# Kernel optimization log

Hardware: AMD Instinct MI355X
Metric: run time of the kernel (lower is better)

The kernel has to match this reference:

```python
import jax, jax.numpy as jnp
import numpy as np

N_NODES = 100000
N_EDGES = 1600000
IN_C = 64
HID = 64


def _glorot(key, shape):
    fan_in, fan_out = shape[1], shape[0]
    lim = (6.0 / (fan_in + fan_out)) ** 0.5
    return jax.random.uniform(key, shape, jnp.float32, -lim, lim)


def setup_inputs() -> dict:
    key = jax.random.key(0)
    ks = jax.random.split(key, 8)
    x = jax.random.normal(ks[0], (N_NODES, IN_C), jnp.float32)
    edge_index = jax.random.randint(ks[1], (2, N_EDGES), 0, N_NODES, jnp.int32)
    return {
        "x": x,
        "edge_index": edge_index,
        # conv1 (SAGEConv in->hid): lin_l (bias), lin_r (no bias)
        "W1l": _glorot(ks[2], (HID, IN_C)),
        "b1l": jnp.zeros((HID,), jnp.float32),
        "W1r": _glorot(ks[3], (HID, IN_C)),
        # conv2 (SAGEConv hid->hid)
        "W2l": _glorot(ks[4], (HID, HID)),
        "b2l": jnp.zeros((HID,), jnp.float32),
        "W2r": _glorot(ks[5], (HID, HID)),
        # edge scorer: Linear(2*hid, 1)
        "Wlin": _glorot(ks[6], (1, 2 * HID)),
        "blin": jnp.zeros((1,), jnp.float32),
    }


def _sage_conv(x, src, dst, Wl, bl, Wr, n_nodes):
    # mean aggregation of source features onto destination nodes
    agg = jax.ops.segment_sum(x[src], dst, num_segments=n_nodes)  # [N, F]
    cnt = jax.ops.segment_sum(jnp.ones((src.shape[0],), x.dtype), dst,
                              num_segments=n_nodes)  # [N]
    mean = agg / jnp.maximum(cnt, 1.0)[:, None]  # isolated nodes -> 0
    return mean @ Wl.T + bl + x @ Wr.T


def reference(x, edge_index, W1l, b1l, W1r, W2l, b2l, W2r, Wlin, blin):
    src, dst = edge_index[0], edge_index[1]
    n = x.shape[0]
    h = jax.nn.relu(_sage_conv(x, src, dst, W1l, b1l, W1r, n))
    h = jax.nn.relu(_sage_conv(h, src, dst, W2l, b2l, W2r, n))
    he = jnp.concatenate([h[src], h[dst]], axis=1)  # [E, 2*HID]
    return (he @ Wlin.T + blin).squeeze(-1)  # [E]
```

## Files before the change

### kernel.cpp

```cpp
#include <hip/hip_runtime.h>
#include <hip/hip_bf16.h>

#define N_NODES 100000
#define N_EDGES 1600000
#define NBUCK 196
#define BCAP 12288
#define CHUNK 4096
#define PART_BLOCKS 391


typedef __hip_bfloat16 bf16;
typedef short short8 __attribute__((ext_vector_type(8)));
typedef float f32x4 __attribute__((ext_vector_type(4)));
typedef unsigned int uint;

__device__ __forceinline__ short f2bs(float f) {
    bf16 h = __float2bfloat16(f);
    short s; __builtin_memcpy(&s, &h, 2); return s;
}
__device__ __forceinline__ float lo_bf(uint w) {
    uint v = w << 16; float f; __builtin_memcpy(&f, &v, 4); return f;
}
__device__ __forceinline__ float hi_bf(uint w) {
    uint v = w & 0xFFFF0000u; float f; __builtin_memcpy(&f, &v, 4); return f;
}
__device__ __forceinline__ uint pack2(float a, float b) {
    return (uint)(unsigned short)f2bs(a) | ((uint)(unsigned short)f2bs(b) << 16);
}
__device__ __forceinline__ short8 cvt8(const float* __restrict__ p) {
    float4 v0 = *(const float4*)p;
    float4 v1 = *(const float4*)(p + 4);
    short8 t;
    t[0] = f2bs(v0.x); t[1] = f2bs(v0.y); t[2] = f2bs(v0.z); t[3] = f2bs(v0.w);
    t[4] = f2bs(v1.x); t[5] = f2bs(v1.y); t[6] = f2bs(v1.z); t[7] = f2bs(v1.w);
    return t;
}
__device__ __forceinline__ short8 load8bf(const bf16* __restrict__ p, long idx) {
    return *(const short8*)((const short*)p + idx);
}

__global__ __launch_bounds__(256) void convert_kernel(
    const float* __restrict__ in, bf16* __restrict__ out, int* __restrict__ gcur)
{
    int i = blockIdx.x * 256 + threadIdx.x;
    float4 v = ((const float4*)in)[i];
    uint2 o;
    o.x = pack2(v.x, v.y);
    o.y = pack2(v.z, v.w);
    ((uint2*)out)[i] = o;
    if (blockIdx.x == 0) gcur[threadIdx.x] = threadIdx.x * BCAP;
}


__global__ __launch_bounds__(256) void partition_kernel(
    const int* __restrict__ src, const int* __restrict__ dst,
    int* __restrict__ gcur, int* __restrict__ pk)
{
    __shared__ int h[256], scn[256], cur[256], gb[256];
    __shared__ int pl[CHUNK];
    __shared__ unsigned char bb[CHUNK];
    int t = threadIdx.x;
    h[t] = 0;
    __syncthreads();
    int e0 = blockIdx.x * CHUNK;
    for (int i = t; i < CHUNK; i += 256) {
        int e = e0 + i;
        if (e < N_EDGES) atomicAdd(&h[dst[e] >> 9], 1);
    }
    __syncthreads();
    scn[t] = h[t];
    __syncthreads();
#pragma unroll
    for (int off = 1; off < 256; off <<= 1) {
        int add = (t >= off) ? scn[t - off] : 0;
        __syncthreads();
        scn[t] += add;
        __syncthreads();
    }
    cur[t] = scn[t] - h[t];
    __syncthreads();
    int cnt_local = scn[255];
    for (int i = t; i < CHUNK; i += 256) {
        int e = e0 + i;
        if (e < N_EDGES) {
            int d = dst[e];
            int b = d >> 9;
            int p = atomicAdd(&cur[b], 1);
            pl[p] = src[e] | ((d & 511) << 17);
            bb[p] = (unsigned char)b;
        }
    }
    __syncthreads();
    if (h[t] > 0) gb[t] = atomicAdd(&gcur[t], h[t]);
    __syncthreads();
    for (int i = t; i < cnt_local; i += 256) {
        int b = bb[i];
        int pos = gb[b] + (i - (scn[b] - h[b]));
        if (pos < (b + 1) * BCAP) pk[pos] = pl[i];
    }
}

__global__ __launch_bounds__(512) void csr_build(
    const int* __restrict__ gcur, const int* __restrict__ pk,
    int* __restrict__ csr, int2* __restrict__ node_range)
{
    __shared__ int deg[512], scn[512], cur[512];
    __shared__ int csr_l[BCAP];
    int t = threadIdx.x;
    int b = blockIdx.x;
    int base = b * BCAP;
    int cnt = gcur[b] - base;
    if (cnt > BCAP) cnt = BCAP;
    deg[t] = 0;
    __syncthreads();
    for (int i = t; i < cnt; i += 512)
        atomicAdd(&deg[pk[base + i] >> 17], 1);
    __syncthreads();
    scn[t] = deg[t];
    __syncthreads();
#pragma unroll
    for (int off = 1; off < 512; off <<= 1) {
        int add = (t >= off) ? scn[t - off] : 0;
        __syncthreads();
        scn[t] += add;
        __syncthreads();
    }
    int excl = scn[t] - deg[t];
    cur[t] = excl;
    int n = (b << 9) + t;
    if (n < N_NODES) node_range[n] = make_int2(base + excl, base + excl + deg[t]);
    __syncthreads();
    for (int i = t; i < cnt; i += 512) {
        int v = pk[base + i];
        int p = atomicAdd(&cur[v >> 17], 1);
        csr_l[p] = v & 0x1FFFF;
    }
    __syncthreads();
    for (int i = t; i < cnt; i += 512)
        csr[base + i] = csr_l[i];
}

__global__ __launch_bounds__(256) void aggregate_mean(
    const bf16* __restrict__ feat, const int2* __restrict__ node_range,
    const int* __restrict__ csr, bf16* __restrict__ mean)
{
    int wave = threadIdx.x >> 6, lane = threadIdx.x & 63;
    int ri = lane >> 3, ci = lane & 7;
    int n = blockIdx.x * 4 + wave;
    if (n >= N_NODES) return;
    int2 rg = node_range[n];
    int beg = rg.x, end = rg.y;
    const uint* fw = (const uint*)feat;
    float acc[8] = {0.f, 0.f, 0.f, 0.f, 0.f, 0.f, 0.f, 0.f};
    int i = beg + ri;
    for (; i + 8 < end; i += 16) {
        int s0 = csr[i], s1 = csr[i + 8];
        uint4 w0 = *(const uint4*)(fw + (long)s0 * 32 + ci * 4);
        uint4 w1 = *(const uint4*)(fw + (long)s1 * 32 + ci * 4);
        acc[0] += lo_bf(w0.x) + lo_bf(w1.x); acc[1] += hi_bf(w0.x) + hi_bf(w1.x);
        acc[2] += lo_bf(w0.y) + lo_bf(w1.y); acc[3] += hi_bf(w0.y) + hi_bf(w1.y);
        acc[4] += lo_bf(w0.z) + lo_bf(w1.z); acc[5] += hi_bf(w0.z) + hi_bf(w1.z);
        acc[6] += lo_bf(w0.w) + lo_bf(w1.w); acc[7] += hi_bf(w0.w) + hi_bf(w1.w);
    }
    if (i < end) {
        int s = csr[i];
        uint4 w = *(const uint4*)(fw + (long)s * 32 + ci * 4);
        acc[0] += lo_bf(w.x); acc[1] += hi_bf(w.x);
        acc[2] += lo_bf(w.y); acc[3] += hi_bf(w.y);
        acc[4] += lo_bf(w.z); acc[5] += hi_bf(w.z);
        acc[6] += lo_bf(w.w); acc[7] += hi_bf(w.w);
    }
#pragma unroll
    for (int m = 8; m < 64; m <<= 1) {
#pragma unroll
        for (int k = 0; k < 8; k++) acc[k] += __shfl_xor(acc[k], m);
    }
    if (ri == 0) {
        int d = end - beg;
        float inv = d > 0 ? 1.0f / (float)d : 0.0f;
        short8 st;
#pragma unroll
        for (int k = 0; k < 8; k++) st[k] = f2bs(acc[k] * inv);
        *(short8*)((short*)mean + (long)n * 64 + ci * 8) = st;
    }
}

__device__ __forceinline__ void load_afrags(
    short8* a, const bf16* __restrict__ mean,
    const bf16* __restrict__ self, int na, int quad)
{
#pragma unroll
    for (int c = 0; c < 2; c++)
        a[c] = load8bf(mean, (long)na * 64 + c * 32 + quad * 8);
#pragma unroll
    for (int c = 0; c < 2; c++)
        a[2 + c] = load8bf(self, (long)na * 64 + c * 32 + quad * 8);
}

__device__ __forceinline__ short8 load_bfrag(
    const float* __restrict__ Wl, const float* __restrict__ Wr,
    int f, int c, int quad)
{
    if (c < 2) return cvt8(Wl + (long)f * 64 + c * 32 + quad * 8);
    return cvt8(Wr + (long)f * 64 + (c - 2) * 32 + quad * 8);
}

__global__ __launch_bounds__(256) void node_layer1_mfma(
    const bf16* __restrict__ xb, const bf16* __restrict__ mean,
    const float* __restrict__ Wl, const float* __restrict__ bl,
    const float* __restrict__ Wr, bf16* __restrict__ h_out)
{
    int tid = threadIdx.x;
    int wave = tid >> 6, lane = tid & 63;
    int quad = lane >> 4, n16 = lane & 15;
    int nb = (blockIdx.x * 4 + wave) * 16;

    int node_a = nb + n16;
    int na = node_a < N_NODES ? node_a : N_NODES - 1;
    short8 a[4];
    load_afrags(a, mean, xb, na, quad);

#pragma unroll
    for (int t = 0; t < 4; t++) {
        int f = 16 * t + n16;
        f32x4 acc = {0.f, 0.f, 0.f, 0.f};
#pragma unroll
        for (int c = 0; c < 4; c++) {
            short8 b = load_bfrag(Wl, Wr, f, c, quad);
            acc = __builtin_amdgcn_mfma_f32_16x16x32_bf16(a[c], b, acc, 0, 0, 0);
        }
        float bias = bl[f];
#pragma unroll
        for (int r = 0; r < 4; r++) {
            int node = nb + quad * 4 + r;
            if (node < N_NODES)
                h_out[(long)node * 64 + f] = __float2bfloat16(fmaxf(acc[r] + bias, 0.0f));
        }
    }
}

__global__ __launch_bounds__(256) void node_layer2_mfma(
    const bf16* __restrict__ h1, const bf16* __restrict__ mean,
    const float* __restrict__ Wl, const float* __restrict__ bl,
    const float* __restrict__ Wr, const float* __restrict__ Wlin,
    float* __restrict__ s_src, float* __restrict__ s_dst)
{
    int tid = threadIdx.x;
    int wave = tid >> 6, lane = tid & 63;
    int quad = lane >> 4, n16 = lane & 15;
    int nb = (blockIdx.x * 4 + wave) * 16;

    int node_a = nb + n16;
    int na = node_a < N_NODES ? node_a : N_NODES - 1;
    short8 a[4];
    load_afrags(a, mean, h1, na, quad);

    float sa[4] = {0.f, 0.f, 0.f, 0.f};
    float sb[4] = {0.f, 0.f, 0.f, 0.f};
#pragma unroll
    for (int t = 0; t < 4; t++) {
        int f = 16 * t + n16;
        f32x4 acc = {0.f, 0.f, 0.f, 0.f};
#pragma unroll
        for (int c = 0; c < 4; c++) {
            short8 b = load_bfrag(Wl, Wr, f, c, quad);
            acc = __builtin_amdgcn_mfma_f32_16x16x32_bf16(a[c], b, acc, 0, 0, 0);
        }
        float bias = bl[f];
        float wa = Wlin[f];
        float wb = Wlin[64 + f];
#pragma unroll
        for (int r = 0; r < 4; r++) {
            float h = fmaxf(acc[r] + bias, 0.0f);
            sa[r] += h * wa;
            sb[r] += h * wb;
        }
    }
#pragma unroll
    for (int m = 1; m < 16; m <<= 1) {
#pragma unroll
        for (int r = 0; r < 4; r++) {
            sa[r] += __shfl_xor(sa[r], m);
            sb[r] += __shfl_xor(sb[r], m);
        }
    }
    if (n16 == 0) {
#pragma unroll
        for (int r = 0; r < 4; r++) {
            int node = nb + quad * 4 + r;
            if (node < N_NODES) { s_src[node] = sa[r]; s_dst[node] = sb[r]; }
        }
    }
}

__global__ __launch_bounds__(256) void edge_out_kernel(
    const int* __restrict__ src, const int* __restrict__ dst,
    const float* __restrict__ s_src, const float* __restrict__ s_dst,
    const float* __restrict__ blin, float* __restrict__ out)
{
    int i = blockIdx.x * 256 + threadIdx.x;
    if (i >= N_EDGES / 4) return;
    int4 s4 = ((const int4*)src)[i];
    int4 d4 = ((const int4*)dst)[i];
    float b = blin[0];
    float4 o;
    o.x = s_src[s4.x] + s_dst[d4.x] + b;
    o.y = s_src[s4.y] + s_dst[d4.y] + b;
    o.z = s_src[s4.z] + s_dst[d4.z] + b;
    o.w = s_src[s4.w] + s_dst[d4.w] + b;
    ((float4*)out)[i] = o;
}

extern "C" void kernel_launch(void* const* d_in, const int* in_sizes, int n_in,
                              void* d_out, int out_size, void* d_ws, size_t ws_size,
                              hipStream_t stream) {
    const float* x    = (const float*)d_in[0];
    const int*   ei   = (const int*)d_in[1];
    const float* W1l  = (const float*)d_in[2];
    const float* b1l  = (const float*)d_in[3];
    const float* W1r  = (const float*)d_in[4];
    const float* W2l  = (const float*)d_in[5];
    const float* b2l  = (const float*)d_in[6];
    const float* W2r  = (const float*)d_in[7];
    const float* Wlin = (const float*)d_in[8];
    const float* blin = (const float*)d_in[9];
    float* out = (float*)d_out;

    const int* src = ei;
    const int* dst = ei + N_EDGES;

    char* w = (char*)d_ws;
    bf16*  xb    = (bf16*)w;  w += (size_t)N_NODES * 64 * 2;
    bf16*  mean  = (bf16*)w;  w += (size_t)N_NODES * 64 * 2;
    bf16*  h1    = (bf16*)w;  w += (size_t)N_NODES * 64 * 2;
    float* ssrc  = (float*)w; w += (size_t)N_NODES * 4;
    float* sdst  = (float*)w; w += (size_t)N_NODES * 4;
    int2*  nrng  = (int2*)w;  w += (size_t)N_NODES * 8;
    int*   gcur  = (int*)w;   w += 256 * 4;
    int*   pk    = (int*)w;   w += (size_t)NBUCK * BCAP * 4;
    int*   csr   = (int*)w;   w += (size_t)NBUCK * BCAP * 4;

    const int conv_blocks = (N_NODES * 64 / 4) / 256;
    const int agg_blocks  = (N_NODES + 3) / 4;
    const int node_blocks = (N_NODES + 63) / 64;
    const int eo_blocks   = (N_EDGES / 4 + 255) / 256;

    convert_kernel<<<conv_blocks, 256, 0, stream>>>(x, xb, gcur);
    partition_kernel<<<PART_BLOCKS, 256, 0, stream>>>(src, dst, gcur, pk);
    csr_build<<<NBUCK, 512, 0, stream>>>(gcur, pk, csr, nrng);

    aggregate_mean<<<agg_blocks, 256, 0, stream>>>(xb, nrng, csr, mean);
    node_layer1_mfma<<<node_blocks, 256, 0, stream>>>(xb, mean, W1l, b1l, W1r, h1);

    aggregate_mean<<<agg_blocks, 256, 0, stream>>>(h1, nrng, csr, mean);
    node_layer2_mfma<<<node_blocks, 256, 0, stream>>>(h1, mean, W2l, b2l, W2r, Wlin, ssrc, sdst);

    edge_out_kernel<<<eo_blocks, 256, 0, stream>>>(src, dst, ssrc, sdst, blin, out);
}
```

Baseline: 281.5 us.

## Assign eight nodes per wave in aggregation and pre-convert weights to bf16

```diff
diff --git a/kernel.cpp b/kernel.cpp
--- a/kernel.cpp
+++ b/kernel.cpp
@@ -27,28 +27,34 @@
 __device__ __forceinline__ uint pack2(float a, float b) {
     return (uint)(unsigned short)f2bs(a) | ((uint)(unsigned short)f2bs(b) << 16);
 }
-__device__ __forceinline__ short8 cvt8(const float* __restrict__ p) {
-    float4 v0 = *(const float4*)p;
-    float4 v1 = *(const float4*)(p + 4);
-    short8 t;
-    t[0] = f2bs(v0.x); t[1] = f2bs(v0.y); t[2] = f2bs(v0.z); t[3] = f2bs(v0.w);
-    t[4] = f2bs(v1.x); t[5] = f2bs(v1.y); t[6] = f2bs(v1.z); t[7] = f2bs(v1.w);
-    return t;
-}
 __device__ __forceinline__ short8 load8bf(const bf16* __restrict__ p, long idx) {
     return *(const short8*)((const short*)p + idx);
 }
 
 __global__ __launch_bounds__(256) void convert_kernel(
-    const float* __restrict__ in, bf16* __restrict__ out, int* __restrict__ gcur)
-{
-    int i = blockIdx.x * 256 + threadIdx.x;
-    float4 v = ((const float4*)in)[i];
-    uint2 o;
-    o.x = pack2(v.x, v.y);
-    o.y = pack2(v.z, v.w);
-    ((uint2*)out)[i] = o;
-    if (blockIdx.x == 0) gcur[threadIdx.x] = threadIdx.x * BCAP;
+    const float* __restrict__ in, bf16* __restrict__ out, int* __restrict__ gcur,
+    const float* __restrict__ W1l, const float* __restrict__ W1r,
+    const float* __restrict__ W2l, const float* __restrict__ W2r,
+    bf16* __restrict__ wb)
+{
+    if (blockIdx.x < 6250) {
+        int i = blockIdx.x * 256 + threadIdx.x;
+        float4 v = ((const float4*)in)[i];
+        uint2 o;
+        o.x = pack2(v.x, v.y);
+        o.y = pack2(v.z, v.w);
+        ((uint2*)out)[i] = o;
+        if (blockIdx.x == 0) gcur[threadIdx.x] = threadIdx.x * BCAP;
+    } else {
+        for (int k = threadIdx.x; k < 16384; k += 256) {
+            float v;
+            if (k < 4096)       v = W1l[k];
+            else if (k < 8192)  v = W1r[k - 4096];
+            else if (k < 12288) v = W2l[k - 8192];
+            else                v = W2r[k - 12288];
+            wb[k] = __float2bfloat16(v);
+        }
+    }
 }
 
 
@@ -145,44 +151,45 @@
     const int* __restrict__ csr, bf16* __restrict__ mean)
 {
     int wave = threadIdx.x >> 6, lane = threadIdx.x & 63;
-    int ri = lane >> 3, ci = lane & 7;
-    int n = blockIdx.x * 4 + wave;
-    if (n >= N_NODES) return;
+    int g = lane >> 3, ci = lane & 7;
+    int n = (blockIdx.x * 4 + wave) * 8 + g;
     int2 rg = node_range[n];
     int beg = rg.x, end = rg.y;
     const uint* fw = (const uint*)feat;
-    float acc[8] = {0.f, 0.f, 0.f, 0.f, 0.f, 0.f, 0.f, 0.f};
-    int i = beg + ri;
-    for (; i + 8 < end; i += 16) {
-        int s0 = csr[i], s1 = csr[i + 8];
+    float a0 = 0.f, a1 = 0.f, a2 = 0.f, a3 = 0.f;
+    float a4 = 0.f, a5 = 0.f, a6 = 0.f, a7 = 0.f;
+    int i = beg;
+    for (; i + 3 < end; i += 4) {
+        int s0 = csr[i], s1 = csr[i + 1], s2 = csr[i + 2], s3 = csr[i + 3];
         uint4 w0 = *(const uint4*)(fw + (long)s0 * 32 + ci * 4);
         uint4 w1 = *(const uint4*)(fw + (long)s1 * 32 + ci * 4);
-        acc[0] += lo_bf(w0.x) + lo_bf(w1.x); acc[1] += hi_bf(w0.x) + hi_bf(w1.x);
-        acc[2] += lo_bf(w0.y) + lo_bf(w1.y); acc[3] += hi_bf(w0.y) + hi_bf(w1.y);
-        acc[4] += lo_bf(w0.z) + lo_bf(w1.z); acc[5] += hi_bf(w0.z) + hi_bf(w1.z);
-        acc[6] += lo_bf(w0.w) + lo_bf(w1.w); acc[7] += hi_bf(w0.w) + hi_bf(w1.w);
-    }
-    if (i < end) {
+        uint4 w2 = *(const uint4*)(fw + (long)s2 * 32 + ci * 4);
+        uint4 w3 = *(const uint4*)(fw + (long)s3 * 32 + ci * 4);
+        a0 += lo_bf(w0.x) + lo_bf(w1.x) + lo_bf(w2.x) + lo_bf(w3.x);
+        a1 += hi_bf(w0.x) + hi_bf(w1.x) + hi_bf(w2.x) + hi_bf(w3.x);
+        a2 += lo_bf(w0.y) + lo_bf(w1.y) + lo_bf(w2.y) + lo_bf(w3.y);
+        a3 += hi_bf(w0.y) + hi_bf(w1.y) + hi_bf(w2.y) + hi_bf(w3.y);
+        a4 += lo_bf(w0.z) + lo_bf(w1.z) + lo_bf(w2.z) + lo_bf(w3.z);
+        a5 += hi_bf(w0.z) + hi_bf(w1.z) + hi_bf(w2.z) + hi_bf(w3.z);
+        a6 += lo_bf(w0.w) + lo_bf(w1.w) + lo_bf(w2.w) + lo_bf(w3.w);
+        a7 += hi_bf(w0.w) + hi_bf(w1.w) + hi_bf(w2.w) + hi_bf(w3.w);
+    }
+    for (; i < end; i++) {
         int s = csr[i];
         uint4 w = *(const uint4*)(fw + (long)s * 32 + ci * 4);
-        acc[0] += lo_bf(w.x); acc[1] += hi_bf(w.x);
-        acc[2] += lo_bf(w.y); acc[3] += hi_bf(w.y);
-        acc[4] += lo_bf(w.z); acc[5] += hi_bf(w.z);
-        acc[6] += lo_bf(w.w); acc[7] += hi_bf(w.w);
-    }
-#pragma unroll
-    for (int m = 8; m < 64; m <<= 1) {
-#pragma unroll
-        for (int k = 0; k < 8; k++) acc[k] += __shfl_xor(acc[k], m);
-    }
-    if (ri == 0) {
-        int d = end - beg;
-        float inv = d > 0 ? 1.0f / (float)d : 0.0f;
-        short8 st;
-#pragma unroll
-        for (int k = 0; k < 8; k++) st[k] = f2bs(acc[k] * inv);
-        *(short8*)((short*)mean + (long)n * 64 + ci * 8) = st;
-    }
+        a0 += lo_bf(w.x); a1 += hi_bf(w.x);
+        a2 += lo_bf(w.y); a3 += hi_bf(w.y);
+        a4 += lo_bf(w.z); a5 += hi_bf(w.z);
+        a6 += lo_bf(w.w); a7 += hi_bf(w.w);
+    }
+    int d = end - beg;
+    float inv = d > 0 ? 1.0f / (float)d : 0.0f;
+    uint4 q;
+    q.x = pack2(a0 * inv, a1 * inv);
+    q.y = pack2(a2 * inv, a3 * inv);
+    q.z = pack2(a4 * inv, a5 * inv);
+    q.w = pack2(a6 * inv, a7 * inv);
+    *(uint4*)((uint*)mean + (long)n * 32 + ci * 4) = q;
 }
 
 __device__ __forceinline__ void load_afrags(
@@ -198,17 +205,16 @@
 }
 
 __device__ __forceinline__ short8 load_bfrag(
-    const float* __restrict__ Wl, const float* __restrict__ Wr,
-    int f, int c, int quad)
-{
-    if (c < 2) return cvt8(Wl + (long)f * 64 + c * 32 + quad * 8);
-    return cvt8(Wr + (long)f * 64 + (c - 2) * 32 + quad * 8);
+    const bf16* __restrict__ wlb, int f, int c, int quad)
+{
+    if (c < 2) return load8bf(wlb, (long)f * 64 + c * 32 + quad * 8);
+    return load8bf(wlb, 4096 + (long)f * 64 + (c - 2) * 32 + quad * 8);
 }
 
 __global__ __launch_bounds__(256) void node_layer1_mfma(
     const bf16* __restrict__ xb, const bf16* __restrict__ mean,
-    const float* __restrict__ Wl, const float* __restrict__ bl,
-    const float* __restrict__ Wr, bf16* __restrict__ h_out)
+    const bf16* __restrict__ wlb, const float* __restrict__ bl,
+    bf16* __restrict__ h_out)
 {
     int tid = threadIdx.x;
     int wave = tid >> 6, lane = tid & 63;
@@ -226,7 +232,7 @@
         f32x4 acc = {0.f, 0.f, 0.f, 0.f};
 #pragma unroll
         for (int c = 0; c < 4; c++) {
-            short8 b = load_bfrag(Wl, Wr, f, c, quad);
+            short8 b = load_bfrag(wlb, f, c, quad);
             acc = __builtin_amdgcn_mfma_f32_16x16x32_bf16(a[c], b, acc, 0, 0, 0);
         }
         float bias = bl[f];
@@ -241,8 +247,8 @@
 
 __global__ __launch_bounds__(256) void node_layer2_mfma(
     const bf16* __restrict__ h1, const bf16* __restrict__ mean,
-    const float* __restrict__ Wl, const float* __restrict__ bl,
-    const float* __restrict__ Wr, const float* __restrict__ Wlin,
+    const bf16* __restrict__ wlb, const float* __restrict__ bl,
+    const float* __restrict__ Wlin,
     float* __restrict__ s_src, float* __restrict__ s_dst)
 {
     int tid = threadIdx.x;
@@ -263,7 +269,7 @@
         f32x4 acc = {0.f, 0.f, 0.f, 0.f};
 #pragma unroll
         for (int c = 0; c < 4; c++) {
-            short8 b = load_bfrag(Wl, Wr, f, c, quad);
+            short8 b = load_bfrag(wlb, f, c, quad);
             acc = __builtin_amdgcn_mfma_f32_16x16x32_bf16(a[c], b, acc, 0, 0, 0);
         }
         float bias = bl[f];
@@ -337,23 +343,24 @@
     float* sdst  = (float*)w; w += (size_t)N_NODES * 4;
     int2*  nrng  = (int2*)w;  w += (size_t)N_NODES * 8;
     int*   gcur  = (int*)w;   w += 256 * 4;
+    bf16*  wb    = (bf16*)w;  w += 16384 * 2;
     int*   pk    = (int*)w;   w += (size_t)NBUCK * BCAP * 4;
     int*   csr   = (int*)w;   w += (size_t)NBUCK * BCAP * 4;
 
-    const int conv_blocks = (N_NODES * 64 / 4) / 256;
-    const int agg_blocks  = (N_NODES + 3) / 4;
+    const int conv_blocks = 6251;
+    const int agg_blocks  = N_NODES / 32;
     const int node_blocks = (N_NODES + 63) / 64;
     const int eo_blocks   = (N_EDGES / 4 + 255) / 256;
 
-    convert_kernel<<<conv_blocks, 256, 0, stream>>>(x, xb, gcur);
+    convert_kernel<<<conv_blocks, 256, 0, stream>>>(x, xb, gcur, W1l, W1r, W2l, W2r, wb);
     partition_kernel<<<PART_BLOCKS, 256, 0, stream>>>(src, dst, gcur, pk);
     csr_build<<<NBUCK, 512, 0, stream>>>(gcur, pk, csr, nrng);
 
     aggregate_mean<<<agg_blocks, 256, 0, stream>>>(xb, nrng, csr, mean);
-    node_layer1_mfma<<<node_blocks, 256, 0, stream>>>(xb, mean, W1l, b1l, W1r, h1);
+    node_layer1_mfma<<<node_blocks, 256, 0, stream>>>(xb, mean, wb, b1l, h1);
 
     aggregate_mean<<<agg_blocks, 256, 0, stream>>>(h1, nrng, csr, mean);
-    node_layer2_mfma<<<node_blocks, 256, 0, stream>>>(h1, mean, W2l, b2l, W2r, Wlin, ssrc, sdst);
+    node_layer2_mfma<<<node_blocks, 256, 0, stream>>>(h1, mean, wb + 8192, b2l, Wlin, ssrc, sdst);
 
     edge_out_kernel<<<eo_blocks, 256, 0, stream>>>(src, dst, ssrc, sdst, blin, out);
 }
```

After: 257.7 us. 8.5% less time.
